# Kernel optimization log

Measured on AMD Instinct MI355X. Metric: run time of the kernel, lower is better.

The kernel has to match this reference:

```python
import jax, jax.numpy as jnp
import numpy as np

EMB_DIM = 2048
NUM_HEADS = 16
HEAD_DIM = 128  # EMB_DIM // NUM_HEADS


def setup_inputs() -> dict:
    key = jax.random.key(0)
    k1, k2, k3 = jax.random.split(key, 3)
    B, T, C = 4, 2048, EMB_DIM
    scale = 1.0 / np.sqrt(C)
    return {
        "x": jax.random.normal(k1, (B, T, C), dtype=jnp.float32),
        "W_qkv": jax.random.normal(k2, (C, 3 * C), dtype=jnp.float32) * scale,
        "b_qkv": jnp.zeros((3 * C,), dtype=jnp.float32),
        "W_proj": jax.random.normal(k3, (C, C), dtype=jnp.float32) * scale,
        "b_proj": jnp.zeros((C,), dtype=jnp.float32),
    }


def reference(x, W_qkv, b_qkv, W_proj, b_proj):
    B, T, C = x.shape
    H, D = NUM_HEADS, HEAD_DIM
    qkv = x @ W_qkv + b_qkv                      # [B,T,3C]
    q, k, v = jnp.split(qkv, 3, axis=-1)         # each [B,T,C]
    # [B,T,C] -> [B,H,T,D]
    q = q.reshape(B, T, H, D).transpose(0, 2, 1, 3)
    k = k.reshape(B, T, H, D).transpose(0, 2, 1, 3)
    v = v.reshape(B, T, H, D).transpose(0, 2, 1, 3)
    scores = jnp.einsum("bhqd,bhkd->bhqk", q, k) / jnp.sqrt(jnp.asarray(D, x.dtype))
    causal = jnp.tril(jnp.ones((T, T), dtype=bool))
    scores = jnp.where(causal, scores, jnp.asarray(-jnp.inf, x.dtype))
    attn = jax.nn.softmax(scores, axis=-1)
    out = jnp.einsum("bhqk,bhkd->bhqd", attn, v)  # [B,H,T,D]
    out = out.transpose(0, 2, 1, 3).reshape(B, T, C)
    return out @ W_proj + b_proj
```

## Files before the change

### kernel.cpp

```cpp
#include <hip/hip_runtime.h>


typedef __bf16 bf16;
typedef __bf16 bf16x8 __attribute__((ext_vector_type(8)));
typedef __bf16 bf16x4 __attribute__((ext_vector_type(4)));
typedef float f32x4 __attribute__((ext_vector_type(4)));

__device__ __forceinline__ void gload_lds16(const void* g, void* l) {
  __builtin_amdgcn_global_load_lds(
      (const __attribute__((address_space(1))) void*)g,
      (__attribute__((address_space(3))) void*)l, 16, 0, 0);
}

__global__ __launch_bounds__(256) void cast_f32_bf16(
    const float* __restrict__ in, bf16* __restrict__ out, int n8) {
  for (int i = blockIdx.x * 256 + threadIdx.x; i < n8; i += gridDim.x * 256) {
    const float4* p = (const float4*)in + (size_t)i * 2;
    float4 a = p[0], b = p[1];
    bf16x8 o8 = {(bf16)a.x, (bf16)a.y, (bf16)a.z, (bf16)a.w,
                 (bf16)b.x, (bf16)b.y, (bf16)b.z, (bf16)b.w};
    *(bf16x8*)(out + (size_t)i * 8) = o8;
  }
}

__global__ __launch_bounds__(256) void transpose_cast(
    const float* __restrict__ in, bf16* __restrict__ out, int R, int C) {
  __shared__ bf16 tile[64 * 64];
  const int r0 = blockIdx.y * 64, c0 = blockIdx.x * 64;
  const int t = threadIdx.x;
  const int ri = t >> 2, cseg = (t & 3) * 16;
  const float4* src =
      (const float4*)&in[(size_t)(r0 + ri) * C + c0 + cseg];
  float4 f0 = src[0], f1 = src[1], f2 = src[2], f3 = src[3];
  bf16x8 h0 = {(bf16)f0.x, (bf16)f0.y, (bf16)f0.z, (bf16)f0.w,
               (bf16)f1.x, (bf16)f1.y, (bf16)f1.z, (bf16)f1.w};
  bf16x8 h1 = {(bf16)f2.x, (bf16)f2.y, (bf16)f2.z, (bf16)f2.w,
               (bf16)f3.x, (bf16)f3.y, (bf16)f3.z, (bf16)f3.w};
  const int kx = (ri & 7) << 3;
  *(bf16x8*)&tile[ri * 64 + (cseg ^ kx)] = h0;
  *(bf16x8*)&tile[ri * 64 + ((cseg + 8) ^ kx)] = h1;
  __syncthreads();
  const int oj = t >> 2, rseg = (t & 3) * 16;
  bf16 v[16];
#pragma unroll
  for (int i = 0; i < 16; ++i) {
    const int rr = rseg + i;
    v[i] = tile[rr * 64 + (oj ^ ((rr & 7) << 3))];
  }
  bf16* dst = &out[(size_t)(c0 + oj) * R + r0 + rseg];
  *(bf16x8*)dst = *(bf16x8*)&v[0];
  *(bf16x8*)(dst + 8) = *(bf16x8*)&v[8];
}

template <int EPI>
__global__ __launch_bounds__(512, 2) void gemm256(
    const bf16* __restrict__ A, const bf16* __restrict__ BT,
    const float* __restrict__ bias, int M, int N, int K,
    float* __restrict__ outf, bf16* __restrict__ qb, bf16* __restrict__ kb,
    bf16* __restrict__ vtb) {
  __shared__ bf16 As[2][2][256 * 32];
  __shared__ bf16 Bs[2][2][256 * 32];
  const int tid = threadIdx.x;
  const int lane = tid & 63, w = tid >> 6;
  const int wm = w >> 2, wn = w & 3;
  const int lr = lane & 15, lg = lane >> 4;

  const int xcd = blockIdx.x & 7, local = blockIdx.x >> 3;
  const int mt = xcd * 4 + (local & 3), nt = local >> 2;
  const int m0 = mt * 256, n0 = nt * 256;

  auto STAGE_H = [&](int d, int skh, int sisB, int kt) {
    const bf16* src = sisB ? BT : A;
    const int r0 = sisB ? n0 : m0;
    bf16* lb = sisB ? &Bs[d][skh][0] : &As[d][skh][0];
#pragma unroll
    for (int c = 0; c < 2; ++c) {
      const int chunk = w * 2 + c;
      const int row = chunk * 16 + (lane >> 2);
      const int col = ((lane & 3) * 8) ^ (((row >> 3) & 1) << 4);
      gload_lds16(src + (size_t)(r0 + row) * K + kt * 64 + skh * 32 + col,
                  (char*)lb + chunk * 1024);
    }
  };
  auto LDA = [&](int d, int kh, int mi) -> bf16x8 {
    const int row = wm * 128 + mi * 16 + lr;
    return *(const bf16x8*)((const char*)&As[d][kh][0] +
                            ((row * 64 + lg * 16) ^ ((lr >> 3) << 5)));
  };
  auto LDB = [&](int d, int kh, int ni) -> bf16x8 {
    const int row = wn * 64 + ni * 16 + lr;
    return *(const bf16x8*)((const char*)&Bs[d][kh][0] +
                            ((row * 64 + lg * 16) ^ ((lr >> 3) << 5)));
  };

  f32x4 acc[8][4] = {};
  const int NT = K >> 6;

  auto COMPUTE = [&](int d, int kh) {
    bf16x8 af[8], bfr[4];
#pragma unroll
    for (int mi = 0; mi < 8; ++mi) af[mi] = LDA(d, kh, mi);
#pragma unroll
    for (int ni = 0; ni < 4; ++ni) bfr[ni] = LDB(d, kh, ni);
#pragma unroll
    for (int mi = 0; mi < 8; ++mi)
#pragma unroll
      for (int ni = 0; ni < 4; ++ni)
        acc[mi][ni] = __builtin_amdgcn_mfma_f32_16x16x32_bf16(
            af[mi], bfr[ni], acc[mi][ni], 0, 0, 0);
  };

  STAGE_H(0, 0, 0, 0);
  STAGE_H(0, 0, 1, 0);
  STAGE_H(0, 1, 0, 0);
  STAGE_H(0, 1, 1, 0);
  asm volatile("s_waitcnt vmcnt(0)" ::: "memory");
  __builtin_amdgcn_s_barrier();

  const int kh_first = (w >> 2) & 1;
  for (int t = 0; t < NT; ++t) {
    const int cur = t & 1;
    if (t + 1 < NT) {
      STAGE_H(cur ^ 1, 0, 0, t + 1);
      STAGE_H(cur ^ 1, 0, 1, t + 1);
      STAGE_H(cur ^ 1, 1, 0, t + 1);
      STAGE_H(cur ^ 1, 1, 1, t + 1);
    }
    __builtin_amdgcn_s_setprio(1);
    COMPUTE(cur, kh_first);
    COMPUTE(cur, kh_first ^ 1);
    __builtin_amdgcn_s_setprio(0);
    asm volatile("s_waitcnt vmcnt(0)" ::: "memory");
    __builtin_amdgcn_s_barrier();
  }

#pragma unroll
  for (int mi = 0; mi < 8; ++mi) {
    const int mbase = m0 + wm * 128 + mi * 16 + lg * 4;
#pragma unroll
    for (int ni = 0; ni < 4; ++ni) {
      const int n = n0 + wn * 64 + ni * 16 + lr;
      const float bv = bias[n];
      if (EPI == 1) {
#pragma unroll
        for (int r = 0; r < 4; ++r)
          outf[(size_t)(mbase + r) * N + n] = acc[mi][ni][r] + bv;
      } else {
        const int which = n >> 11;
        const int cc = n & 2047, h = cc >> 7, dd = cc & 127;
        const int b = mbase >> 11, t0 = mbase & 2047;
        const int bh = b * 16 + h;
        if (which == 2) {
          bf16x4 pk;
#pragma unroll
          for (int r = 0; r < 4; ++r) pk[r] = (bf16)(acc[mi][ni][r] + bv);
          *(bf16x4*)&vtb[((size_t)bh * 128 + dd) * 2048 + t0] = pk;
        } else {
          bf16* dst = (which == 0) ? qb : kb;
#pragma unroll
          for (int r = 0; r < 4; ++r)
            dst[((size_t)bh * 2048 + t0 + r) * 128 + dd] =
                (bf16)(acc[mi][ni][r] + bv);
        }
      }
    }
  }
}

__global__ __launch_bounds__(512) void attn_kernel(
    const bf16* __restrict__ qb, const bf16* __restrict__ kb,
    const bf16* __restrict__ vtb, bf16* __restrict__ ob) {
  __shared__ bf16 Ks[2][128 * 128];
  __shared__ bf16 Vs[2][128 * 128];
  __shared__ bf16 Ps[8][16 * 64];
  const int tid = threadIdx.x, lane = tid & 63, w = tid >> 6;
  const int bh = blockIdx.y;
  const int qtA = blockIdx.x;
  const int qtB = 15 - qtA;
  const int qt_w = (w < 4) ? qtA : qtB;
  const int wq = w & 3;
  const int lr = lane & 15, lg = lane >> 4;
  const int q0 = qt_w * 128;
  const size_t base = (size_t)bh * (2048 * 128);
  const int rswz = (lr & 7) << 3;

  const float qscale = 0.08838834764831845f * 1.4426950408889634f;
  bf16x8 qf[2][4];
#pragma unroll
  for (int g = 0; g < 2; ++g) {
    const bf16* qp =
        qb + base + (size_t)(q0 + g * 64 + wq * 16 + lr) * 128 + lg * 8;
#pragma unroll
    for (int kk = 0; kk < 4; ++kk) {
      bf16x8 t = *(const bf16x8*)(qp + kk * 32);
#pragma unroll
      for (int e = 0; e < 8; ++e) t[e] = (bf16)((float)t[e] * qscale);
      qf[g][kk] = t;
    }
  }

  f32x4 o[2][8] = {};
  float mst[2] = {-1e30f, -1e30f};
  float lst[2] = {0.f, 0.f};

  auto STAGE = [&](int bsel, int kt) {
#pragma unroll
    for (int c = 0; c < 4; ++c) {
      const int off = w * 1024 + c * 8192 + lane * 16;
      const int row = off >> 8, ce = (off & 255) >> 1;
      gload_lds16(kb + base + (size_t)(kt * 128 + row) * 128 +
                      (ce ^ ((row & 7) << 3)),
                  (char*)Ks[bsel] + w * 1024 + c * 8192);
      gload_lds16(vtb + base + (size_t)row * 2048 + kt * 128 +
                      (ce ^ ((row & 7) << 3)),
                  (char*)Vs[bsel] + w * 1024 + c * 8192);
    }
  };

  const int nst = qtB + 1;
  STAGE(0, 0);
  for (int kt = 0; kt < nst; ++kt) {
    const int cur = kt & 1;
    if (kt + 1 < nst) {
      STAGE(cur ^ 1, kt + 1);
      asm volatile("s_waitcnt vmcnt(8)" ::: "memory");
    } else {
      asm volatile("s_waitcnt vmcnt(0)" ::: "memory");
    }
    __builtin_amdgcn_s_barrier();
    __builtin_amdgcn_sched_barrier(0);

    const bf16* Kc = Ks[cur];
    const bf16* Vc = Vs[cur];
#pragma unroll
    for (int g = 0; g < 2; ++g) {
      const int gb = 2 * qt_w + g;
      const int gbrel = gb - 2 * kt;
      if (gbrel < 0) continue;

      f32x4 s[8] = {};
      __builtin_amdgcn_s_setprio(1);
#pragma unroll
      for (int kk = 0; kk < 4; ++kk)
#pragma unroll
        for (int j = 0; j < 8; ++j) {
          const bf16x8 kf = *(const bf16x8*)&Kc[(j * 16 + lr) * 128 +
                                               ((kk * 32 + lg * 8) ^ rswz)];
          s[j] = __builtin_amdgcn_mfma_f32_16x16x32_bf16(kf, qf[g][kk], s[j],
                                                         0, 0, 0);
        }
      __builtin_amdgcn_s_setprio(0);

      if (gbrel <= 1) {
        const int qq = gbrel * 64 + wq * 16 + lr;
#pragma unroll
        for (int j = 0; j < 8; ++j)
#pragma unroll
          for (int r = 0; r < 4; ++r)
            if (j * 16 + lg * 4 + r > qq) s[j][r] = -1e30f;
      }

      float pm;
      {
        float a0 = -1e30f, a1 = -1e30f;
#pragma unroll
        for (int j = 0; j < 8; j += 2) {
          a0 = fmaxf(a0, fmaxf(fmaxf(s[j][0], s[j][1]),
                               fmaxf(s[j][2], s[j][3])));
          a1 = fmaxf(a1, fmaxf(fmaxf(s[j + 1][0], s[j + 1][1]),
                               fmaxf(s[j + 1][2], s[j + 1][3])));
        }
        pm = fmaxf(a0, a1);
      }
      pm = fmaxf(pm, __shfl_xor(pm, 16));
      pm = fmaxf(pm, __shfl_xor(pm, 32));

      if (__any(pm > mst[g] + 8.0f)) {
        const float mnew = fmaxf(mst[g], pm);
        const float alpha = __builtin_amdgcn_exp2f(mst[g] - mnew);
        mst[g] = mnew;
        lst[g] *= alpha;
#pragma unroll
        for (int r = 0; r < 4; ++r) {
          const float av = __shfl(alpha, (lane & 48) | (lg * 4 + r));
#pragma unroll
          for (int n = 0; n < 8; ++n) o[g][n][r] *= av;
        }
      }

      float rs = 0.f;
#pragma unroll
      for (int j = 0; j < 8; ++j)
#pragma unroll
        for (int r = 0; r < 4; ++r) {
          const float p = __builtin_amdgcn_exp2f(s[j][r] - mst[g]);
          s[j][r] = p;
          rs += p;
        }
      rs += __shfl_xor(rs, 16);
      rs += __shfl_xor(rs, 32);
      lst[g] += rs;

      __builtin_amdgcn_s_setprio(1);
#pragma unroll
      for (int h = 0; h < 2; ++h) {
#pragma unroll
        for (int j2 = 0; j2 < 4; ++j2) {
          const int j = h * 4 + j2;
          bf16x4 pw;
#pragma unroll
          for (int r = 0; r < 4; ++r) pw[r] = (bf16)s[j][r];
          *(bf16x4*)&Ps[w][lr * 64 + ((j2 * 16 + lg * 4) ^ rswz)] = pw;
        }
        bf16x8 pf[2];
#pragma unroll
        for (int kk = 0; kk < 2; ++kk)
          pf[kk] = *(const bf16x8*)&Ps[w][lr * 64 +
                                         ((kk * 32 + lg * 8) ^ rswz)];
#pragma unroll
        for (int n = 0; n < 8; ++n)
#pragma unroll
          for (int kk = 0; kk < 2; ++kk) {
            const bf16x8 vf = *(const bf16x8*)&Vc[(n * 16 + lr) * 128 +
                                                 ((h * 64 + kk * 32 +
                                                   lg * 8) ^ rswz)];
            o[g][n] = __builtin_amdgcn_mfma_f32_16x16x32_bf16(
                pf[kk], vf, o[g][n], 0, 0, 0);
          }
      }
      __builtin_amdgcn_s_setprio(0);
    }
    __builtin_amdgcn_sched_barrier(0);
    __builtin_amdgcn_s_barrier();
    __builtin_amdgcn_sched_barrier(0);
  }

  const int b = bh >> 4, h = bh & 15;
#pragma unroll
  for (int g = 0; g < 2; ++g)
#pragma unroll
    for (int r = 0; r < 4; ++r) {
      const float inv = 1.0f / __shfl(lst[g], (lane & 48) | (lg * 4 + r));
      const int t = q0 + g * 64 + wq * 16 + lg * 4 + r;
      bf16* dst = ob + ((size_t)(b * 2048 + t)) * 2048 + h * 128;
#pragma unroll
      for (int n = 0; n < 8; ++n) dst[n * 16 + lr] = (bf16)(o[g][n][r] * inv);
    }
}

extern "C" void kernel_launch(void* const* d_in, const int* in_sizes, int n_in,
                              void* d_out, int out_size, void* d_ws,
                              size_t ws_size, hipStream_t stream) {
  const float* x = (const float*)d_in[0];
  const float* Wqkv = (const float*)d_in[1];
  const float* bqkv = (const float*)d_in[2];
  const float* Wproj = (const float*)d_in[3];
  const float* bproj = (const float*)d_in[4];
  float* out = (float*)d_out;

  char* ws = (char*)d_ws;
  bf16* xb     = (bf16*)(ws);
  bf16* wqkvT  = (bf16*)(ws + 33554432);
  bf16* wprojT = (bf16*)(ws + 58720256);
  bf16* qb     = (bf16*)(ws + 67108864);
  bf16* kb     = (bf16*)(ws + 100663296);
  bf16* vtb    = (bf16*)(ws + 134217728);
  bf16* ab     = (bf16*)(ws + 167772160);

  cast_f32_bf16<<<2048, 256, 0, stream>>>(x, xb, 2097152);
  transpose_cast<<<dim3(96, 32), 256, 0, stream>>>(Wqkv, wqkvT, 2048, 6144);
  transpose_cast<<<dim3(32, 32), 256, 0, stream>>>(Wproj, wprojT, 2048, 2048);
  gemm256<0><<<768, 512, 0, stream>>>(xb, wqkvT, bqkv, 8192, 6144, 2048,
                                      nullptr, qb, kb, vtb);
  attn_kernel<<<dim3(8, 64), 512, 0, stream>>>(qb, kb, vtb, ab);
  gemm256<1><<<256, 512, 0, stream>>>(ab, wprojT, bproj, 8192, 2048, 2048,
                                      out, nullptr, nullptr, nullptr);
}
```

Baseline: 512.4 us.

## Interleave GEMM global-to-LDS staging with MFMA phases at half-tile granularity

Restructures the 256x256 GEMM main loop into eight phases per two K-tiles. Each phase loads half the A fragments, issues one quarter-tile global-to-LDS stage, then runs 16 MFMAs, with barriers and partial vmcnt waits in place of one full drain per K-tile. The aim is to overlap memory traffic with compute more finely and cut the stall at each tile boundary. It adds many more barriers per tile and a complex buffer-reuse schedule, and it assumes NT is even.

```diff
diff --git a/kernel.cpp b/kernel.cpp
--- a/kernel.cpp
+++ b/kernel.cpp
@@ -69,10 +69,10 @@
   const int mt = xcd * 4 + (local & 3), nt = local >> 2;
   const int m0 = mt * 256, n0 = nt * 256;
 
-  auto STAGE_H = [&](int d, int skh, int sisB, int kt) {
+  auto STAGE_H = [&](int skh, int sisB, int kt) {
     const bf16* src = sisB ? BT : A;
     const int r0 = sisB ? n0 : m0;
-    bf16* lb = sisB ? &Bs[d][skh][0] : &As[d][skh][0];
+    bf16* lb = sisB ? &Bs[kt & 1][skh][0] : &As[kt & 1][skh][0];
 #pragma unroll
     for (int c = 0; c < 2; ++c) {
       const int chunk = w * 2 + c;
@@ -94,44 +94,54 @@
   };
 
   f32x4 acc[8][4] = {};
+  bf16x8 bfr[4];
   const int NT = K >> 6;
 
-  auto COMPUTE = [&](int d, int kh) {
-    bf16x8 af[8], bfr[4];
-#pragma unroll
-    for (int mi = 0; mi < 8; ++mi) af[mi] = LDA(d, kh, mi);
-#pragma unroll
-    for (int ni = 0; ni < 4; ++ni) bfr[ni] = LDB(d, kh, ni);
-#pragma unroll
-    for (int mi = 0; mi < 8; ++mi)
+  auto PHASE = [&](int d, int kh, int mh, int st, int skh, int sB, int vm) {
+    if (mh == 0) {
+#pragma unroll
+      for (int ni = 0; ni < 4; ++ni) bfr[ni] = LDB(d, kh, ni);
+    }
+    bf16x8 af4[4];
+#pragma unroll
+    for (int j = 0; j < 4; ++j) af4[j] = LDA(d, kh, mh * 4 + j);
+    if (st < NT) STAGE_H(skh, sB, st);
+    __builtin_amdgcn_s_barrier();
+    asm volatile("s_waitcnt lgkmcnt(0)" ::: "memory");
+    __builtin_amdgcn_sched_barrier(0);
+    __builtin_amdgcn_s_setprio(1);
+#pragma unroll
+    for (int j = 0; j < 4; ++j)
 #pragma unroll
       for (int ni = 0; ni < 4; ++ni)
-        acc[mi][ni] = __builtin_amdgcn_mfma_f32_16x16x32_bf16(
-            af[mi], bfr[ni], acc[mi][ni], 0, 0, 0);
-  };
-
-  STAGE_H(0, 0, 0, 0);
-  STAGE_H(0, 0, 1, 0);
-  STAGE_H(0, 1, 0, 0);
-  STAGE_H(0, 1, 1, 0);
-  asm volatile("s_waitcnt vmcnt(0)" ::: "memory");
+        acc[mh * 4 + j][ni] = __builtin_amdgcn_mfma_f32_16x16x32_bf16(
+            af4[j], bfr[ni], acc[mh * 4 + j][ni], 0, 0, 0);
+    __builtin_amdgcn_s_setprio(0);
+    if (vm == 4) asm volatile("s_waitcnt vmcnt(4)" ::: "memory");
+    else if (vm == 0) asm volatile("s_waitcnt vmcnt(0)" ::: "memory");
+    __builtin_amdgcn_s_barrier();
+  };
+
+  STAGE_H(0, 0, 0);
+  STAGE_H(0, 1, 0);
+  STAGE_H(1, 0, 0);
+  STAGE_H(1, 1, 0);
+  STAGE_H(0, 0, 1);
+  STAGE_H(0, 1, 1);
+  asm volatile("s_waitcnt vmcnt(4)" ::: "memory");
   __builtin_amdgcn_s_barrier();
 
-  const int kh_first = (w >> 2) & 1;
-  for (int t = 0; t < NT; ++t) {
-    const int cur = t & 1;
-    if (t + 1 < NT) {
-      STAGE_H(cur ^ 1, 0, 0, t + 1);
-      STAGE_H(cur ^ 1, 0, 1, t + 1);
-      STAGE_H(cur ^ 1, 1, 0, t + 1);
-      STAGE_H(cur ^ 1, 1, 1, t + 1);
-    }
-    __builtin_amdgcn_s_setprio(1);
-    COMPUTE(cur, kh_first);
-    COMPUTE(cur, kh_first ^ 1);
-    __builtin_amdgcn_s_setprio(0);
-    asm volatile("s_waitcnt vmcnt(0)" ::: "memory");
-    __builtin_amdgcn_s_barrier();
+  for (int a = 0; a < NT; a += 2) {
+    const int b = a + 1;
+    const bool p34 = (a + 2 < NT);
+    PHASE(0, 0, 0, b, 1, 0, -1);
+    PHASE(0, 0, 1, b, 1, 1, -1);
+    PHASE(0, 1, 0, a + 2, 0, 0, -1);
+    PHASE(0, 1, 1, a + 2, 0, 1, p34 ? 4 : 0);
+    PHASE(1, 0, 0, a + 2, 1, 0, -1);
+    PHASE(1, 0, 1, a + 2, 1, 1, -1);
+    PHASE(1, 1, 0, b + 2, 0, 0, -1);
+    PHASE(1, 1, 1, b + 2, 0, 1, p34 ? 4 : 0);
   }
 
 #pragma unroll
```

Measured after the change: 457.1 us. 10.8% less time.
